# Kernel tuning notes

Measured on AMD Instinct MI355X. Metric: run time of the kernel, lower is better.

Reference implementation:

```python
import jax, jax.numpy as jnp
import numpy as np

B, T_PREV, T_CUR = 256, 128, 129
N_COV, N_TREAT, N_CONF = 30, 57, 5
H, FC = 128, 128
D_IN = N_COV + N_TREAT            # 87, lstm external input size
D_CELL = D_IN + N_CONF            # 92, cell input = [x_t, z_{t-1}]


def setup_inputs() -> dict:
    key = jax.random.key(0)
    ks = jax.random.split(key, 18)
    s = 0.05
    return {
        "previous_covariates": jax.random.normal(ks[0], (B, T_PREV, N_COV), jnp.float32),
        "previous_treatments": jax.random.normal(ks[1], (B, T_PREV, N_TREAT), jnp.float32),
        "current_covariates": jax.random.normal(ks[2], (B, T_CUR, N_COV), jnp.float32),
        "init_input": jax.random.normal(ks[3], (1, 1, D_IN), jnp.float32) * s,
        "h0": jax.random.normal(ks[4], (1, H), jnp.float32) * s,
        "c0": jax.random.normal(ks[5], (1, H), jnp.float32) * s,
        "z0": jax.random.normal(ks[6], (1, N_CONF), jnp.float32) * s,
        "W_ih": jax.random.normal(ks[7], (4 * H, D_CELL), jnp.float32) * s,
        "W_hh": jax.random.normal(ks[8], (4 * H, H), jnp.float32) * s,
        "b_ih": jax.random.normal(ks[9], (4 * H,), jnp.float32) * s,
        "b_hh": jax.random.normal(ks[10], (4 * H,), jnp.float32) * s,
        "W_z": jax.random.normal(ks[11], (N_CONF, H), jnp.float32) * s,
        "b_z": jax.random.normal(ks[12], (N_CONF,), jnp.float32) * s,
        "dec_W1": jax.random.normal(ks[13], (N_TREAT, N_COV + N_CONF, FC), jnp.float32) * s,
        "dec_b1": jax.random.normal(ks[14], (N_TREAT, FC), jnp.float32) * s,
        "dec_W2": jax.random.normal(ks[15], (N_TREAT, FC), jnp.float32) * s,
        "dec_b2": jax.random.normal(ks[16], (N_TREAT,), jnp.float32) * s,
    }


def _forward(previous_covariates, previous_treatments, current_covariates,
             init_input, h0, c0, z0, W_ih, W_hh, b_ih, b_hh, W_z, b_z,
             dec_W1, dec_b1, dec_W2, dec_b2):
    Bn = previous_covariates.shape[0]
    # (T_PREV, B, D_IN)
    x = jnp.concatenate([previous_covariates, previous_treatments], -1).transpose(1, 0, 2)
    # prepend trainable init input -> (T_CUR, B, D_IN)
    rnn_in = jnp.concatenate([jnp.broadcast_to(init_input, (1, Bn, D_IN)), x], 0)

    bias = b_ih + b_hh

    def step(carry, xt):
        h, c, z = carry
        inp = jnp.concatenate([xt, z], -1)                 # (B, D_CELL)
        gates = inp @ W_ih.T + h @ W_hh.T + bias           # (B, 4H)
        i, f, g, o = jnp.split(gates, 4, axis=-1)          # torch LSTMCell gate order
        c = jax.nn.sigmoid(f) * c + jax.nn.sigmoid(i) * jnp.tanh(g)
        h = jax.nn.sigmoid(o) * jnp.tanh(c)
        z = h @ W_z.T + b_z                                # (B, N_CONF)
        return (h, c, z), z

    carry0 = (jnp.broadcast_to(h0, (Bn, H)),
              jnp.broadcast_to(c0, (Bn, H)),
              jnp.broadcast_to(z0, (Bn, N_CONF)))
    _, zs = jax.lax.scan(step, carry0, rnn_in)             # (T_CUR, B, N_CONF)

    hidden_confounders = zs.reshape(-1, N_CONF)            # (T_CUR*B, N_CONF)
    covariates = current_covariates.transpose(1, 0, 2).reshape(-1, N_COV)
    # shapes match by construction (T_CUR*B rows each) -> no pad branch
    multitask_input = jnp.concatenate([hidden_confounders, covariates], -1)  # (N, 35)

    # batched per-treatment Linear -> LeakyReLU(0.01) -> Linear
    hdec = jax.nn.leaky_relu(
        jnp.einsum('nc,tcf->ntf', multitask_input, dec_W1) + dec_b1, 0.01)
    preds = jnp.einsum('ntf,tf->nt', hdec, dec_W2) + dec_b2                   # (N, 57)

    # T_CUR*B % (T_PREV) == 0 with these shapes -> no element trim
    confounders = hidden_confounders.reshape(T_PREV, -1, N_CONF)              # (128, 258, 5)
    return preds, confounders


def reference(previous_covariates, previous_treatments, current_covariates,
              init_input, h0, c0, z0, W_ih, W_hh, b_ih, b_hh, W_z, b_z,
              dec_W1, dec_b1, dec_W2, dec_b2):
    return _forward(previous_covariates, previous_treatments, current_covariates,
                    init_input, h0, c0, z0, W_ih, W_hh, b_ih, b_hh, W_z, b_z,
                    dec_W1, dec_b1, dec_W2, dec_b2)
```

## Files before the change

### kernel.cpp

```cpp
#include <hip/hip_runtime.h>
#include <stdint.h>

#define BATCH 256
#define T_PREVN 128
#define T_CURN 129
#define N_COV 30
#define N_TREAT 57
#define N_CONF 5
#define HID 128
#define D_IN 87
#define D_CELL 92
#define GATES 512
#define PRED_N (T_CURN*BATCH)
#define CONF_OFF (PRED_N*N_TREAT)

#define OFF_W1   0
#define SZ_W1    (57*8*2*64*8*2)
#define OFF_WIH  SZ_W1
#define SZ_WIH   (32*3*64*8*2)
#define OFF_GX   (OFF_W1 + SZ_W1 + SZ_WIH)
#define SZ_GX    (PRED_N*512*2)
#define OFF_MT   (OFF_GX + SZ_GX)
#define SZ_MT    (PRED_N*40*2)
#define WS_GX    (OFF_MT + SZ_MT)
#define WS_NEED  SZ_W1
#define WS_NEED2 (SZ_W1 + SZ_MT)

typedef _Float16 h2 __attribute__((ext_vector_type(2)));
typedef _Float16 h4 __attribute__((ext_vector_type(4)));
typedef _Float16 h8 __attribute__((ext_vector_type(8)));
typedef float f32x4 __attribute__((ext_vector_type(4)));

__device__ inline float rcp_fast(float x){
#if __has_builtin(__builtin_amdgcn_rcpf)
    return __builtin_amdgcn_rcpf(x);
#else
    return 1.0f / x;
#endif
}
__device__ inline float sigmoid_f(float x){ return rcp_fast(1.0f + __expf(-x)); }
__device__ inline float tanh_f(float x){ return 1.0f - 2.0f*rcp_fast(1.0f + __expf(2.0f*x)); }

__device__ inline float dot2f(h2 a, h2 b, float c){
#if __has_builtin(__builtin_amdgcn_fdot2)
    return __builtin_amdgcn_fdot2(a, b, c, false);
#else
    return c + (float)a.x*(float)b.x + (float)a.y*(float)b.y;
#endif
}
__device__ inline unsigned short f2us(float v){
    _Float16 h = (_Float16)v;
    return __builtin_bit_cast(unsigned short, h);
}
__device__ inline h2 us2h2(unsigned int u){
    return __builtin_bit_cast(h2, u);
}

__global__ __launch_bounds__(256) void prep_all(
    const float* __restrict__ dW1, const float* __restrict__ W_ih,
    const float* __restrict__ cc,
    _Float16* __restrict__ wsh, _Float16* __restrict__ wihf,
    _Float16* __restrict__ mT)
{
    const int bid = blockIdx.x;
    if (bid < 228){
        const int tid = bid*256 + threadIdx.x;
        const int treat = tid >> 10;
        const int r     = tid & 1023;
        const int ft    = r >> 7;
        const int ks    = (r >> 6) & 1;
        const int l     = r & 63;
        const int col   = ft*16 + (l & 15);
        const int kb    = ks*32 + ((l >> 4) << 3);
        h8 v;
        #pragma unroll
        for (int j = 0; j < 8; j++){
            const int k = kb + j;
            v[j] = (k < 35) ? (_Float16)dW1[(treat*35 + k)*128 + col] : (_Float16)0.0f;
        }
        *(h8*)(wsh + (size_t)tid*8) = v;
    } else if (bid < 252){
        const int tid = (bid - 228)*256 + threadIdx.x;
        const int ct  = tid / 192;
        const int rem = tid - ct*192;
        const int ks  = rem >> 6;
        const int l   = rem & 63;
        const int gate = ct*16 + (l & 15);
        const int kb   = ks*32 + ((l >> 4) << 3);
        h8 v;
        #pragma unroll
        for (int j = 0; j < 8; j++){
            const int k = kb + j;
            v[j] = (k < D_IN) ? (_Float16)W_ih[gate*D_CELL + k] : (_Float16)0.0f;
        }
        *(h8*)(wihf + (size_t)tid*8) = v;
    } else {
        const int idx = (bid - 252)*256 + threadIdx.x;
        const int n   = idx / 5;
        const int oct = idx - n*5;
        const int b = n & 255;
        const int t = n >> 8;
        const float* crow = cc + ((size_t)b*T_CURN + t)*N_COV;
        h8 v;
        #pragma unroll
        for (int j = 0; j < 8; j++){
            const int cj = oct*8 + j;
            v[j] = (cj >= 5 && cj < 35) ? (_Float16)crow[cj - 5] : (_Float16)0.0f;
        }
        *(h8*)(mT + (size_t)n*40 + oct*8) = v;
    }
}

__global__ __launch_bounds__(256, 2) void gx_gemm(
    const float* __restrict__ pc, const float* __restrict__ pt,
    const float* __restrict__ init_input,
    const _Float16* __restrict__ wihf, _Float16* __restrict__ Gx)
{
    __shared__ alignas(16) _Float16 a_lds[64*104];
    __shared__ alignas(16) _Float16 gx_lds[64*264];

    const int tid = threadIdx.x;
    const int nb  = blockIdx.x * 64;

    for (int idx = tid; idx < 64*96; idx += 256){
        const int r = idx / 96;
        const int k = idx - r*96;
        const int n = nb + r;
        const int bb = n / 129;
        const int t  = n - bb*129;
        float v = 0.0f;
        if (k < D_IN){
            if (t == 0) v = init_input[k];
            else        v = (k < N_COV) ? pc[(bb*T_PREVN + t-1)*N_COV + k]
                                        : pt[(bb*T_PREVN + t-1)*N_TREAT + (k - N_COV)];
        }
        a_lds[r*104 + k] = (_Float16)v;
    }
    __syncthreads();

    const int w    = tid >> 6;
    const int l    = tid & 63;
    const int col  = l & 15;
    const int quad = l >> 4;

    const _Float16* ar = a_lds + (w*16 + col)*104 + quad*8;
    const h8 a0 = *(const h8*)(ar);
    const h8 a1 = *(const h8*)(ar + 32);
    const h8 a2 = *(const h8*)(ar + 64);

    for (int half = 0; half < 2; half++){
        #pragma unroll
        for (int ct8 = 0; ct8 < 16; ct8++){
            const int ct = half*16 + ct8;
            const _Float16* bp = wihf + (size_t)ct*1536 + l*8;
            const h8 b0 = *(const h8*)(bp);
            const h8 b1 = *(const h8*)(bp + 512);
            const h8 b2 = *(const h8*)(bp + 1024);
            f32x4 acc = {0.f, 0.f, 0.f, 0.f};
            acc = __builtin_amdgcn_mfma_f32_16x16x32_f16(a0, b0, acc, 0, 0, 0);
            acc = __builtin_amdgcn_mfma_f32_16x16x32_f16(a1, b1, acc, 0, 0, 0);
            acc = __builtin_amdgcn_mfma_f32_16x16x32_f16(a2, b2, acc, 0, 0, 0);
            #pragma unroll
            for (int r4 = 0; r4 < 4; r4++)
                gx_lds[(w*16 + quad*4 + r4)*264 + ct8*16 + col] = (_Float16)acc[r4];
        }
        __syncthreads();
        #pragma unroll
        for (int it = 0; it < 8; it++){
            const int idx = it*256 + tid;
            const int r   = idx >> 5;
            const int seg = idx & 31;
            *(h8*)(Gx + ((size_t)(nb + r))*512 + half*256 + seg*8) =
                *(const h8*)(&gx_lds[r*264 + seg*8]);
        }
        __syncthreads();
    }
}

__global__ __launch_bounds__(1024, 4) void lstm_scan_oct(
    const float* __restrict__ h0, const float* __restrict__ c0,
    const float* __restrict__ z0,
    const float* __restrict__ W_ih, const float* __restrict__ W_hh,
    const float* __restrict__ b_ih, const float* __restrict__ b_hh,
    const float* __restrict__ W_z, const float* __restrict__ b_z,
    const _Float16* __restrict__ Gx,
    float* __restrict__ zs_out, _Float16* __restrict__ mT)
{
    const int b   = blockIdx.x;
    const int tid = threadIdx.x;
    const int u   = tid >> 3;
    const int r   = tid & 7;
    const int gsel = r >> 1;
    const int gate_l = (gsel << 7) + u;

    __shared__ alignas(16) unsigned short v16h[2][128];
    __shared__ alignas(16) unsigned short hall[T_CURN*136];
    __shared__ alignas(16) unsigned short gxc[2][16*512];
    __shared__ alignas(16) float wzf[5*HID];
    __shared__ alignas(16) _Float16 wz16[5*HID];
    __shared__ float z0c[5];

    for (int i = tid; i < 5*HID; i += 1024){
        const float v = W_z[i];
        wzf[i]  = v;
        wz16[i] = (_Float16)v;
    }
    if (tid < HID) v16h[0][tid] = f2us(h0[tid]);
    if (tid < 5){
        float acc0 = 0.0f, acc1 = 0.0f;
        #pragma unroll 8
        for (int k = 0; k < HID; k += 2){
            acc0 += W_z[tid*HID + k]     * h0[k];
            acc1 += W_z[tid*HID + k + 1] * h0[k + 1];
        }
        z0c[tid] = z0[tid] - b_z[tid] - (acc0 + acc1);
    }
    {
        const int row = tid >> 6;
        const uint4 p = *(const uint4*)(Gx + ((size_t)b*T_CURN + row)*512 + (size_t)(tid & 63)*8);
        *(uint4*)(&gxc[0][(row << 9) + (tid & 63)*8]) = p;
    }
    __syncthreads();

    const int kbase = r << 4;
    h2 wi_[8], wf_[8], wg_[8], wo_[8];
    {
        float zA[5], zB[5], zC[5], zD[5];
        #pragma unroll
// ... 91 lines not shown

        gval += (t == 0) ? b0_l : be_l;
        gval += (float)*(const _Float16*)(&gxc[cb][((t & 15) << 9) + gate_l]);

        const float earg = (gsel == 2) ? (2.0f*gval) : (-gval);
        const float e = __expf(earg);
        const float dd = rcp_fast(1.0f + e);
        const float av = (gsel == 2) ? (1.0f - 2.0f*dd) : dd;

        const float v1 = __shfl_xor(av, 2);
        const float v2 = __shfl_xor(av, 4);
        const float v3 = __shfl_xor(v1, 4);
        float si, sf, tg, so;
        if (gsel == 0){ si = av; sf = v1; tg = v2; so = v3; }
        else if (gsel == 1){ si = v1; sf = av; tg = v3; so = v2; }
        else if (gsel == 2){ si = v2; sf = v3; tg = av; so = v1; }
        else              { si = v3; sf = v2; tg = v1; so = av; }

        c = sf*c + si*tg;
        const float h = so * tanh_f(c);

        if (r == 0){
            const unsigned short hu = f2us(h);
            v16h[(t + 1) & 1][u] = hu;
            hall[t*136 + u] = hu;
        }
        if (pok)
            *(uint4*)(&gxc[cb ^ 1][((tid >> 6) << 9) + (tid & 63)*8]) = pre;
        __syncthreads();
    }

    for (int idx = tid; idx < T_CURN*N_CONF; idx += 1024){
        const int t  = idx / 5;
        const int zi = idx - t*5;
        const uint4* hr = (const uint4*)(hall + t*136);
        const uint4* wr = (const uint4*)(wz16 + zi*HID);
        float s0 = 0.f, s1 = 0.f;
        #pragma unroll
        for (int i = 0; i < 16; i++){
            const uint4 hq = hr[i];
            const uint4 wq = wr[i];
            s0 = dot2f(us2h2(hq.x), us2h2(wq.x), s0);
            s1 = dot2f(us2h2(hq.y), us2h2(wq.y), s1);
            s0 = dot2f(us2h2(hq.z), us2h2(wq.z), s0);
            s1 = dot2f(us2h2(hq.w), us2h2(wq.w), s1);
        }
        const float z = s0 + s1 + b_z[zi];
        const int n = t*BATCH + b;
        zs_out[(size_t)n*N_CONF + zi] = z;
        if (mT) mT[(size_t)n*40 + zi] = (_Float16)z;
    }
}

__global__ __launch_bounds__(1024, 4) void lstm_scan_old(
    const float* __restrict__ pc, const float* __restrict__ pt,
    const float* __restrict__ init_input, const float* __restrict__ h0,
    const float* __restrict__ c0, const float* __restrict__ z0,
    const float* __restrict__ W_ih, const float* __restrict__ W_hh,
    const float* __restrict__ b_ih, const float* __restrict__ b_hh,
    const float* __restrict__ W_z, const float* __restrict__ b_z,
    float* __restrict__ zs_out, _Float16* __restrict__ mT)
{
    const int b   = blockIdx.x;
    const int tid = threadIdx.x;
    const int g   = tid >> 1;
    const int hf  = tid & 1;

    __shared__ alignas(16) unsigned short v16[224];
    __shared__ alignas(16) unsigned short xall[T_CURN*88];
    __shared__ alignas(16) unsigned short hall[T_CURN*136];
    __shared__ alignas(16) float gbuf[GATES];
    __shared__ alignas(16) _Float16 wz16[5*HID];
    __shared__ float z0c[5];

    float wzg[5];
    #pragma unroll
    for (int z = 0; z < 5; z++) wzg[z] = W_ih[g*D_CELL + 87 + z];

    float be = b_ih[g] + b_hh[g];
    #pragma unroll
    for (int z = 0; z < 5; z++) be += wzg[z] * b_z[z];

    h2 w[56];
    if (hf == 0){
        #pragma unroll
        for (int i = 0; i < 43; i++){
            h2 p; p.x = (_Float16)W_ih[g*D_CELL + 2*i];
                  p.y = (_Float16)W_ih[g*D_CELL + 2*i + 1];
            w[i] = p;
        }
        { h2 p; p.x = (_Float16)W_ih[g*D_CELL + 86]; p.y = (_Float16)0.0f; w[43] = p; }
        #pragma unroll
        for (int i = 44; i < 56; i++){
            const int u = 2*(i - 44);
            float f0 = W_hh[g*HID + u], f1 = W_hh[g*HID + u + 1];
            #pragma unroll
            for (int z = 0; z < 5; z++){
                f0 += wzg[z]*W_z[z*HID + u];
                f1 += wzg[z]*W_z[z*HID + u + 1];
            }
            h2 p; p.x = (_Float16)f0; p.y = (_Float16)f1;
            w[i] = p;
        }
    } else {
        #pragma unroll
        for (int i = 0; i < 52; i++){
            const int u = 24 + 2*i;
            float f0 = W_hh[g*HID + u], f1 = W_hh[g*HID + u + 1];
            #pragma unroll
            for (int z = 0; z < 5; z++){
                f0 += wzg[z]*W_z[z*HID + u];
                f1 += wzg[z]*W_z[z*HID + u + 1];
            }
            h2 p; p.x = (_Float16)f0; p.y = (_Float16)f1;
            w[i] = p;
        }
        #pragma unroll
        for (int i = 52; i < 56; i++){ h2 p; p.x=(_Float16)0.f; p.y=(_Float16)0.f; w[i]=p; }
    }

    for (int idx = tid; idx < T_CURN*88; idx += 1024){
        const int row = idx / 88;
        const int col = idx - row*88;
        float v = 0.0f;
        if (col < D_IN){
            if (row == 0) v = init_input[col];
            else {
                const int tp = row - 1;
                v = (col < N_COV) ? pc[(b*T_PREVN + tp)*N_COV + col]
                                  : pt[(b*T_PREVN + tp)*N_TREAT + (col - N_COV)];
            }
        }
        xall[idx] = f2us(v);
    }

    float c = 0.0f;
    if (tid < HID){ v16[88 + tid] = f2us(h0[tid]); c = c0[tid]; }
    if (tid >= 216 && tid < 224) v16[tid] = 0;

    if (tid < 5){
        float acc0 = 0.0f, acc1 = 0.0f;
        #pragma unroll 8
        for (int u = 0; u < HID; u += 2){
            acc0 += W_z[tid*HID + u]     * h0[u];
            acc1 += W_z[tid*HID + u + 1] * h0[u + 1];
        }
        z0c[tid] = z0[tid] - b_z[tid] - (acc0 + acc1);
    }
    __syncthreads();

    if (tid >= 128 && tid < 216) v16[tid - 128] = xall[tid - 128];
    float b0 = be;
    #pragma unroll
    for (int z = 0; z < 5; z++) b0 += wzg[z] * z0c[z];
    __syncthreads();

    const unsigned short* vbase = v16 + hf*112;
    for (int t = 0; t < T_CURN; t++){
        float a0 = 0.f, a1 = 0.f, a2 = 0.f, a3 = 0.f;
        #pragma unroll
        for (int i = 0; i < 14; i++){
            const uint4 q = *(const uint4*)(vbase + i*8);
            a0 = dot2f(w[4*i+0], us2h2(q.x), a0);
            a1 = dot2f(w[4*i+1], us2h2(q.y), a1);
            a2 = dot2f(w[4*i+2], us2h2(q.z), a2);
            a3 = dot2f(w[4*i+3], us2h2(q.w), a3);
        }
        float s = (a0 + a1) + (a2 + a3);
        s += __shfl_xor(s, 1);
        if (hf == 0) gbuf[g] = s + ((t == 0) ? b0 : be);
        __syncthreads();

        if (tid < HID){
            const float gi = gbuf[tid];
            const float gf = gbuf[128 + tid];
            const float gg = gbuf[256 + tid];
            const float go = gbuf[384 + tid];
            c = sigmoid_f(gf)*c + sigmoid_f(gi)*tanh_f(gg);
            const float h = sigmoid_f(go)*tanh_f(c);
            const unsigned short hu = f2us(h);
            v16[88 + tid] = hu;
            hall[t*136 + tid] = hu;
        } else if (tid < 216){
            if (t < T_PREVN) v16[tid - 128] = xall[(t + 1)*88 + (tid - 128)];
        }
        __syncthreads();
    }

    for (int i = tid; i < 5*HID; i += 1024) wz16[i] = (_Float16)W_z[i];
    __syncthreads();

    if (tid < T_CURN*N_CONF){
        const int t  = tid / 5;
        const int zi = tid - t*5;
        const uint4* hr = (const uint4*)(hall + t*136);
        const uint4* wr = (const uint4*)(wz16 + zi*HID);
        float a0 = 0.f, a1 = 0.f;
        #pragma unroll
        for (int i = 0; i < 16; i++){
            const uint4 hq = hr[i];
            const uint4 wq = wr[i];
            a0 = dot2f(us2h2(hq.x), us2h2(wq.x), a0);
            a1 = dot2f(us2h2(hq.y), us2h2(wq.y), a1);
            a0 = dot2f(us2h2(hq.z), us2h2(wq.z), a0);
            a1 = dot2f(us2h2(hq.w), us2h2(wq.w), a1);
        }
        const float z = a0 + a1 + b_z[zi];
        const int n = t*BATCH + b;
        zs_out[(size_t)n*N_CONF + zi] = z;
        if (mT) mT[(size_t)n*40 + zi] = (_Float16)z;
    }
}

__global__ __launch_bounds__(256) void prepack_w1(const float* __restrict__ dW1,
                                                  _Float16* __restrict__ wsh)
{
    const int tid = blockIdx.x*256 + threadIdx.x;
    const int treat = tid >> 10;
    const int r     = tid & 1023;
    const int ft    = r >> 7;
    const int ks    = (r >> 6) & 1;
    const int l     = r & 63;
    const int col   = ft*16 + (l & 15);
    const int kb    = ks*32 + ((l >> 4) << 3);
    h8 v;
    #pragma unroll
    for (int j = 0; j < 8; j++){
        const int k = kb + j;
        v[j] = (k < 35) ? (_Float16)dW1[(treat*35 + k)*128 + col] : (_Float16)0.0f;
    }
    *(h8*)(wsh + (size_t)tid*8) = v;
}

__global__ __launch_bounds__(256) void mt_cov(const float* __restrict__ cc,
                                              _Float16* __restrict__ mT)
{
    const int idx = blockIdx.x*256 + threadIdx.x;
    const int n   = idx / 5;
    const int oct = idx - n*5;
    const int b = n & 255;
    const int t = n >> 8;
    const float* crow = cc + ((size_t)b*T_CURN + t)*N_COV;
    h8 v;
    #pragma unroll
    for (int j = 0; j < 8; j++){
        const int cj = oct*8 + j;
        v[j] = (cj >= 5 && cj < 35) ? (_Float16)crow[cj - 5] : (_Float16)0.0f;
    }
    *(h8*)(mT + (size_t)n*40 + oct*8) = v;
}

__global__ __launch_bounds__(256, 2) void decoder_treat(
    const _Float16* __restrict__ mT, const _Float16* __restrict__ wsh,
    const float* __restrict__ db1, const float* __restrict__ dW2,
    const float* __restrict__ db2, float* __restrict__ preds)
{
    const int treat = blockIdx.x;
    const int rg    = blockIdx.y;
    const int w     = threadIdx.x >> 6;
    const int l     = threadIdx.x & 63;
    const int q     = l >> 4;
    const int r16   = l & 15;

    h8 bf0[8], bf1[8];
    const _Float16* bp = wsh + (size_t)treat*8192 + l*8;
    #pragma unroll
    for (int ft = 0; ft < 8; ft++){
        bf0[ft] = *(const h8*)(bp + ft*1024);
        bf1[ft] = *(const h8*)(bp + ft*1024 + 512);
    }
    float b1r[8], w2r[8], w2c[8];
    #pragma unroll
    for (int ft = 0; ft < 8; ft++){
        b1r[ft] = db1[treat*128 + ft*16 + r16];
        w2r[ft] = dW2[treat*128 + ft*16 + r16];
        w2c[ft] = 0.01f * w2r[ft];
    }
    const float b2 = db2[treat];

    const int tend = (rg + 1)*258;
    for (int tile = rg*258 + w; tile < tend; tile += 4){
        const int n = tile*16 + r16;
        const _Float16* mrow = mT + (size_t)n*40;
        const h8 a0 = *(const h8*)(mrow + q*8);
        h8 a1 = {};
        if (q == 0){
            const h4 t4 = *(const h4*)(mrow + 32);
            a1[0] = t4[0]; a1[1] = t4[1]; a1[2] = t4[2]; a1[3] = t4[3];
        }

        f32x4 pred = {0.f, 0.f, 0.f, 0.f};
        #pragma unroll
        for (int ft = 0; ft < 8; ft++){
            f32x4 acc = {b1r[ft], b1r[ft], b1r[ft], b1r[ft]};
            acc = __builtin_amdgcn_mfma_f32_16x16x32_f16(a0, bf0[ft], acc, 0, 0, 0);
            acc = __builtin_amdgcn_mfma_f32_16x16x32_f16(a1, bf1[ft], acc, 0, 0, 0);
            #pragma unroll
            for (int r = 0; r < 4; r++){
                const float a  = acc[r];
                const float mx = fmaxf(a, 0.0f);
                const float mn = fminf(a, 0.0f);
                pred[r] += mx*w2r[ft] + mn*w2c[ft];
            }
        }
        #pragma unroll
        for (int r = 0; r < 4; r++){
            float s = pred[r];
            s += __shfl_xor(s, 1);
            s += __shfl_xor(s, 2);
            s += __shfl_xor(s, 4);
            s += __shfl_xor(s, 8);
            pred[r] = s;
        }
        if (r16 == 0){
            #pragma unroll
            for (int r = 0; r < 4; r++)
                preds[(size_t)(tile*16 + q*4 + r)*N_TREAT + treat] = pred[r] + b2;
        }
    }
}

__global__ __launch_bounds__(256) void decoder_mfma(
    const float* __restrict__ cc, const float* __restrict__ zs,
    const _Float16* __restrict__ wsh,
    const float* __restrict__ db1, const float* __restrict__ dW2,
    const float* __restrict__ db2, float* __restrict__ preds)
{
    __shared__ alignas(16) _Float16 m_lds[64*72];

    const int tid  = threadIdx.x;
    const int base = blockIdx.x * 64;
    const int t    = base >> 8;

    for (int idx = tid; idx < 64*72; idx += 256){
        const int r = idx / 72;
        const int j = idx - r*72;
        const int n = base + r;
        const int b = n & 255;
        float v = 0.0f;
        if (j < 5)       v = zs[n*N_CONF + j];
        else if (j < 35) v = cc[(b*T_CURN + t)*N_COV + (j - 5)];
        m_lds[r*72 + j] = (_Float16)v;
    }
    __syncthreads();

    const int w    = tid >> 6;
    const int l    = tid & 63;
    const int row  = l & 15;
    const int quad = l >> 4;

    const _Float16* arow = m_lds + (w*16 + row)*72 + quad*8;
    const h8 a0 = *(const h8*)(arow);
    const h8 a1 = *(const h8*)(arow + 32);
    const int nbase = base + w*16 + quad*4;

    for (int treat = 0; treat < 57; treat++){
        const _Float16* bp = wsh + (size_t)treat*8192 + l*8;
        f32x4 pred = {0.0f, 0.0f, 0.0f, 0.0f};
        #pragma unroll
        for (int ft = 0; ft < 8; ft++){
            const h8 b0 = *(const h8*)(bp + ft*1024);
            const h8 b1 = *(const h8*)(bp + ft*1024 + 512);
            f32x4 acc = {0.0f, 0.0f, 0.0f, 0.0f};
            acc = __builtin_amdgcn_mfma_f32_16x16x32_f16(a0, b0, acc, 0, 0, 0);
            acc = __builtin_amdgcn_mfma_f32_16x16x32_f16(a1, b1, acc, 0, 0, 0);
            const int col = ft*16 + row;
            const float hb1 = db1[treat*128 + col];
            const float hw2 = dW2[treat*128 + col];
            #pragma unroll
            for (int r = 0; r < 4; r++){
                float hd = acc[r] + hb1;
                hd = (hd > 0.0f) ? hd : 0.01f*hd;
                pred[r] += hd * hw2;
            }
        }
        #pragma unroll
        for (int r = 0; r < 4; r++){
            float s = pred[r];
            s += __shfl_xor(s, 1);
            s += __shfl_xor(s, 2);
            s += __shfl_xor(s, 4);
            s += __shfl_xor(s, 8);
            pred[r] = s;
        }
        if (row == 0){
            const float b2 = db2[treat];
            #pragma unroll
            for (int r = 0; r < 4; r++)
                preds[(size_t)(nbase + r)*N_TREAT + treat] = pred[r] + b2;
        }
    }
}

__global__ __launch_bounds__(256) void decoder_fallback(
    const float* __restrict__ cc, const float* __restrict__ zs,
    const float* __restrict__ dW1, const float* __restrict__ db1,
    const float* __restrict__ dW2, const float* __restrict__ db2,
    float* __restrict__ preds)
{
    const int t     = blockIdx.x;
    const int treat = blockIdx.y;
    const int tid   = threadIdx.x;

    __shared__ alignas(16) float w1t[128*36];
    __shared__ float b1s[128];
    __shared__ float w2s[128];

    for (int it = tid; it < 35*128; it += 256){
        const int cidx = it >> 7;
        const int f    = it & 127;
        w1t[f*36 + cidx] = dW1[(treat*35 + cidx)*128 + f];
    }
    if (tid < 128){
        b1s[tid] = db1[treat*128 + tid];
        w2s[tid] = dW2[treat*128 + tid];
        w1t[tid*36 + 35] = 0.0f;
    }
    __syncthreads();

    const int n = t*BATCH + tid;
    float m[36];
    #pragma unroll
    for (int j = 0; j < N_CONF; j++) m[j] = zs[n*N_CONF + j];
    #pragma unroll
    for (int j = 0; j < N_COV; j++)  m[N_CONF + j] = cc[(tid*T_CURN + t)*N_COV + j];
    m[35] = 0.0f;

    const float b2 = db2[treat];
    float pred = 0.0f;
    for (int f = 0; f < 128; f++){
        float a = b1s[f];
        const float4* wr = (const float4*)(w1t + f*36);
        #pragma unroll
        for (int cq = 0; cq < 9; cq++){
            const float4 v = wr[cq];
            a += m[cq*4+0]*v.x + m[cq*4+1]*v.y + m[cq*4+2]*v.z + m[cq*4+3]*v.w;
        }
        a = (a > 0.0f) ? a : 0.01f*a;
        pred += a * w2s[f];
    }
    preds[n*N_TREAT + treat] = pred + b2;
}

extern "C" void kernel_launch(void* const* d_in, const int* in_sizes, int n_in,
                              void* d_out, int out_size, void* d_ws, size_t ws_size,
                              hipStream_t stream)
{
    const float* pc   = (const float*)d_in[0];
    const float* pt   = (const float*)d_in[1];
    const float* cc   = (const float*)d_in[2];
    const float* init = (const float*)d_in[3];
    const float* h0   = (const float*)d_in[4];
    const float* c0   = (const float*)d_in[5];
    const float* z0   = (const float*)d_in[6];
    const float* W_ih = (const float*)d_in[7];
    const float* W_hh = (const float*)d_in[8];
    const float* b_ih = (const float*)d_in[9];
    const float* b_hh = (const float*)d_in[10];
    const float* W_z  = (const float*)d_in[11];
    const float* b_z  = (const float*)d_in[12];
    const float* dW1  = (const float*)d_in[13];
    const float* db1  = (const float*)d_in[14];
    const float* dW2  = (const float*)d_in[15];
    const float* db2  = (const float*)d_in[16];

    float* preds = (float*)d_out;
    float* zs    = (float*)d_out + CONF_OFF;

    if (ws_size >= (size_t)WS_GX){
        _Float16* wsh  = (_Float16*)d_ws;
        _Float16* wihf = (_Float16*)((char*)d_ws + OFF_WIH);
        _Float16* Gx   = (_Float16*)((char*)d_ws + OFF_GX);
        _Float16* mT   = (_Float16*)((char*)d_ws + OFF_MT);

        prep_all<<<897, 256, 0, stream>>>(dW1, W_ih, cc, wsh, wihf, mT);
        gx_gemm<<<516, 256, 0, stream>>>(pc, pt, init, wihf, Gx);
        lstm_scan_oct<<<BATCH, 1024, 0, stream>>>(h0, c0, z0, W_ih, W_hh,
                                                  b_ih, b_hh, W_z, b_z, Gx, zs, mT);
        decoder_treat<<<dim3(N_TREAT, 8), 256, 0, stream>>>(mT, wsh, db1, dW2, db2, preds);
    } else if (ws_size >= (size_t)WS_NEED2){
        _Float16* wsh = (_Float16*)d_ws;
        _Float16* mT  = (_Float16*)((char*)d_ws + WS_NEED);
        prepack_w1<<<228, 256, 0, stream>>>(dW1, wsh);
        mt_cov<<<645, 256, 0, stream>>>(cc, mT);
        lstm_scan_old<<<BATCH, 1024, 0, stream>>>(pc, pt, init, h0, c0, z0,
                                                  W_ih, W_hh, b_ih, b_hh, W_z, b_z, zs, mT);
        decoder_treat<<<dim3(N_TREAT, 8), 256, 0, stream>>>(mT, wsh, db1, dW2, db2, preds);
    } else if (ws_size >= (size_t)WS_NEED){
        _Float16* wsh = (_Float16*)d_ws;
        prepack_w1<<<228, 256, 0, stream>>>(dW1, wsh);
        lstm_scan_old<<<BATCH, 1024, 0, stream>>>(pc, pt, init, h0, c0, z0,
                                                  W_ih, W_hh, b_ih, b_hh, W_z, b_z,
                                                  zs, (_Float16*)nullptr);
        decoder_mfma<<<516, 256, 0, stream>>>(cc, zs, wsh, db1, dW2, db2, preds);
    } else {
        lstm_scan_old<<<BATCH, 1024, 0, stream>>>(pc, pt, init, h0, c0, z0,
                                                  W_ih, W_hh, b_ih, b_hh, W_z, b_z,
                                                  zs, (_Float16*)nullptr);
        decoder_fallback<<<dim3(T_CURN, N_TREAT), 256, 0, stream>>>(
            cc, zs, dW1, db1, dW2, db2, preds);
    }
}
```

Baseline: 233.0 us.

## Batch 16 sequences per block in LSTM scan using MFMA recurrence

Adds an LSTM scan kernel in which each block processes 16 batch rows and computes the recurrent h·W_eff product with MFMA. The input gate contributions from Gx are prefetched through a triple-buffered LDS ring, and z is computed by an extra MFMA on one wave. Bias and initial-confounder terms are folded into the Gx GEMM epilogue, and W_eff plus W_z are prepacked into fragment layout in prep_all. Only 16 blocks are launched instead of 256, which trades parallelism across CUs for tensor-core throughput on the serial recurrence.

```diff
diff --git a/kernel.cpp b/kernel.cpp
--- a/kernel.cpp
+++ b/kernel.cpp
@@ -23,6 +23,11 @@
 #define OFF_MT   (OFF_GX + SZ_GX)
 #define SZ_MT    (PRED_N*40*2)
 #define WS_GX    (OFF_MT + SZ_MT)
+#define OFF_WEFF WS_GX
+#define SZ_WEFF  (32*4*64*8*2)
+#define OFF_WZF  (OFF_WEFF + SZ_WEFF)
+#define SZ_WZF   (4*64*8*2)
+#define WS_MF    (OFF_WZF + SZ_WZF)
 #define WS_NEED  SZ_W1
 #define WS_NEED2 (SZ_W1 + SZ_MT)
 
@@ -58,9 +63,11 @@
 
 __global__ __launch_bounds__(256) void prep_all(
     const float* __restrict__ dW1, const float* __restrict__ W_ih,
-    const float* __restrict__ cc,
+    const float* __restrict__ cc, const float* __restrict__ W_hh,
+    const float* __restrict__ W_z,
     _Float16* __restrict__ wsh, _Float16* __restrict__ wihf,
-    _Float16* __restrict__ mT)
+    _Float16* __restrict__ mT, _Float16* __restrict__ weff,
+    _Float16* __restrict__ wzfr)
 {
     const int bid = blockIdx.x;
     if (bid < 228){
@@ -94,7 +101,7 @@
             v[j] = (k < D_IN) ? (_Float16)W_ih[gate*D_CELL + k] : (_Float16)0.0f;
         }
         *(h8*)(wihf + (size_t)tid*8) = v;
-    } else {
+    } else if (bid < 897){
         const int idx = (bid - 252)*256 + threadIdx.x;
         const int n   = idx / 5;
         const int oct = idx - n*5;
@@ -108,16 +115,58 @@
             v[j] = (cj >= 5 && cj < 35) ? (_Float16)crow[cj - 5] : (_Float16)0.0f;
         }
         *(h8*)(mT + (size_t)n*40 + oct*8) = v;
+    } else if (bid < 929){
+        const int idx = (bid - 897)*256 + threadIdx.x;
+        const int mk  = idx >> 6;
+        const int l   = idx & 63;
+        const int m   = mk >> 2;
+        const int ks  = mk & 3;
+        const int rowp = m*16 + (l & 15);
+        const int u   = rowp >> 2;
+        const int gi  = rowp & 3;
+        const int g   = gi*128 + u;
+        const int kb  = ks*32 + ((l >> 4) << 3);
+        float wz[5];
+        #pragma unroll
+        for (int z = 0; z < 5; z++) wz[z] = W_ih[g*D_CELL + D_IN + z];
+        h8 v;
+        #pragma unroll
+        for (int j = 0; j < 8; j++){
+            const int k = kb + j;
+            float f = W_hh[g*HID + k];
+            #pragma unroll
+            for (int z = 0; z < 5; z++) f += wz[z]*W_z[z*HID + k];
+            v[j] = (_Float16)f;
+        }
+        *(h8*)(weff + (size_t)idx*8) = v;
+    } else {
+        const int t2 = threadIdx.x;
+        const int ks = t2 >> 6;
+        const int l  = t2 & 63;
+        const int row = l & 15;
+        const int kb  = ks*32 + ((l >> 4) << 3);
+        h8 v;
+        #pragma unroll
+        for (int j = 0; j < 8; j++)
+            v[j] = (row < 5) ? (_Float16)W_z[row*HID + kb + j] : (_Float16)0.0f;
+        *(h8*)(wzfr + (size_t)t2*8) = v;
     }
 }
 
 __global__ __launch_bounds__(256, 2) void gx_gemm(
     const float* __restrict__ pc, const float* __restrict__ pt,
     const float* __restrict__ init_input,
-    const _Float16* __restrict__ wihf, _Float16* __restrict__ Gx)
+    const _Float16* __restrict__ wihf, _Float16* __restrict__ Gx,
+    const float* __restrict__ W_ih, const float* __restrict__ W_z,
+    const float* __restrict__ b_ih, const float* __restrict__ b_hh,
+    const float* __restrict__ b_z, const float* __restrict__ h0,
+    const float* __restrict__ z0, const int fold_bias)
 {
     __shared__ alignas(16) _Float16 a_lds[64*104];
     __shared__ alignas(16) _Float16 gx_lds[64*264];
+    __shared__ float be_lds[512];
+    __shared__ float d0_lds[512];
+    __shared__ float z0c[5];
 
     const int tid = threadIdx.x;
     const int nb  = blockIdx.x * 64;
@@ -136,7 +185,29 @@
         }
         a_lds[r*104 + k] = (_Float16)v;
     }
+    if (fold_bias && tid < 5){
+        float a0 = 0.f, a1 = 0.f;
+        #pragma unroll 8
+        for (int k = 0; k < HID; k += 2){
+            a0 += W_z[tid*HID + k]     * h0[k];
+            a1 += W_z[tid*HID + k + 1] * h0[k + 1];
+        }
+        z0c[tid] = z0[tid] - b_z[tid] - (a0 + a1);
+    }
     __syncthreads();
+    if (fold_bias){
+        for (int g = tid; g < 512; g += 256){
+            float w0v = W_ih[g*D_CELL + D_IN + 0];
+            float w1v = W_ih[g*D_CELL + D_IN + 1];
+            float w2v = W_ih[g*D_CELL + D_IN + 2];
+            float w3v = W_ih[g*D_CELL + D_IN + 3];
+            float w4v = W_ih[g*D_CELL + D_IN + 4];
+            be_lds[g] = b_ih[g] + b_hh[g]
+                      + w0v*b_z[0] + w1v*b_z[1] + w2v*b_z[2] + w3v*b_z[3] + w4v*b_z[4];
+            d0_lds[g] = w0v*z0c[0] + w1v*z0c[1] + w2v*z0c[2] + w3v*z0c[3] + w4v*z0c[4];
+        }
+        __syncthreads();
+    }
 
     const int w    = tid >> 6;
     const int l    = tid & 63;
@@ -161,8 +232,16 @@
             acc = __builtin_amdgcn_mfma_f32_16x16x32_f16(a1, b1, acc, 0, 0, 0);
             acc = __builtin_amdgcn_mfma_f32_16x16x32_f16(a2, b2, acc, 0, 0, 0);
             #pragma unroll
-            for (int r4 = 0; r4 < 4; r4++)
-                gx_lds[(w*16 + quad*4 + r4)*264 + ct8*16 + col] = (_Float16)acc[r4];
+            for (int r4 = 0; r4 < 4; r4++){
+                float val = acc[r4];
+                if (fold_bias){
+                    const int g = ct*16 + col;
+                    const int n = nb + w*16 + quad*4 + r4;
+                    val += be_lds[g];
+                    if (n % 129 == 0) val += d0_lds[g];
+                }
+                gx_lds[(w*16 + quad*4 + r4)*264 + ct8*16 + col] = (_Float16)val;
+            }
         }
         __syncthreads();
         #pragma unroll
@@ -174,6 +253,140 @@
                 *(const h8*)(&gx_lds[r*264 + seg*8]);
         }
         __syncthreads();
+    }
+}
+
+__global__ __launch_bounds__(1024, 4) void lstm_scan_mfma(
+    const float* __restrict__ h0, const float* __restrict__ c0,
+    const float* __restrict__ b_z,
+    const _Float16* __restrict__ weff, const _Float16* __restrict__ wzfr,
+    const _Float16* __restrict__ Gx,
+    float* __restrict__ zs_out, _Float16* __restrict__ mT)
+{
+    const int tid = threadIdx.x;
+    const int w   = tid >> 6;
+    const int l   = tid & 63;
+    const int col = l & 15;
+    const int q   = l >> 4;
+    const int b0  = blockIdx.x * 16;
+
+    __shared__ alignas(16) _Float16 hsw[2][16*128];
+    __shared__ alignas(16) _Float16 gxc[3][16*520];
+    __shared__ float zl[129*80];
+
+    for (int idx = tid; idx < 2048; idx += 1024){
+        const int bt = idx >> 7;
+        const int u  = idx & 127;
+        const int gp = (u >> 3) ^ (bt & 7);
+        hsw[0][bt*128 + gp*8 + (u & 7)] = (_Float16)h0[u];
+    }
+    {
+        const uint4 p = *(const uint4*)(Gx + ((size_t)(b0 + w)*T_CURN + 0)*512 + (size_t)l*8);
+        *(uint4*)(&gxc[0][w*520 + l*8]) = p;
+    }
+    uint4 preA = *(const uint4*)(Gx + ((size_t)(b0 + w)*T_CURN + 1)*512 + (size_t)l*8);
+
+    h8 aw0[4], aw1[4], az[4];
+    #pragma unroll
+    for (int ks = 0; ks < 4; ks++){
+        aw0[ks] = *(const h8*)(weff + (size_t)((w*4 + ks)*64 + l)*8);
+        aw1[ks] = *(const h8*)(weff + (size_t)(((w + 16)*4 + ks)*64 + l)*8);
+        az[ks]  = *(const h8*)(wzfr + (size_t)(ks*64 + l)*8);
+    }
+    const int u0 = 4*w + q;
+    const int u1 = 64 + 4*w + q;
+    float cr0 = c0[u0];
+    float cr1 = c0[u1];
+    __syncthreads();
+
+    for (int t = 0; t < T_CURN; t++){
+        const int cur  = t & 1;
+        const int g3   = t % 3;
+        uint4 preB;
+        const bool ldB = (t + 2 <= 128);
+        if (ldB)
+            preB = *(const uint4*)(Gx + ((size_t)(b0 + w)*T_CURN + (t + 2))*512 + (size_t)l*8);
+
+        f32x4 acc0 = {0.f,0.f,0.f,0.f};
+        f32x4 acc1 = {0.f,0.f,0.f,0.f};
+        f32x4 accz = {0.f,0.f,0.f,0.f};
+        #pragma unroll
+        for (int ks = 0; ks < 4; ks++){
+            const int gp = (ks*4 + q) ^ (col & 7);
+            const h8 hb = *(const h8*)(&hsw[cur][col*128 + gp*8]);
+            acc0 = __builtin_amdgcn_mfma_f32_16x16x32_f16(aw0[ks], hb, acc0, 0, 0, 0);
+            acc1 = __builtin_amdgcn_mfma_f32_16x16x32_f16(aw1[ks], hb, acc1, 0, 0, 0);
+            if (w == 15)
+                accz = __builtin_amdgcn_mfma_f32_16x16x32_f16(az[ks], hb, accz, 0, 0, 0);
+        }
+
+        float g0[4], g1[4];
+        #pragma unroll
+        for (int r = 0; r < 4; r++){
+            g0[r] = acc0[r] + (float)gxc[g3][col*520 + r*128 + u0];
+            g1[r] = acc1[r] + (float)gxc[g3][col*520 + r*128 + u1];
+        }
+        float hv0, hv1;
+        {
+            const float i_ = sigmoid_f(g0[0]);
+            const float f_ = sigmoid_f(g0[1]);
+            const float t_ = tanh_f(g0[2]);
+            const float o_ = sigmoid_f(g0[3]);
+            cr0 = f_*cr0 + i_*t_;
+            hv0 = o_ * tanh_f(cr0);
+        }
+        {
+            const float i_ = sigmoid_f(g1[0]);
+            const float f_ = sigmoid_f(g1[1]);
+            const float t_ = tanh_f(g1[2]);
+            const float o_ = sigmoid_f(g1[3]);
+            cr1 = f_*cr1 + i_*t_;
+            hv1 = o_ * tanh_f(cr1);
+        }
+        {
+            const int gp0 = (u0 >> 3) ^ (col & 7);
+            hsw[cur ^ 1][col*128 + gp0*8 + (u0 & 7)] = (_Float16)hv0;
+            const int gp1 = (u1 >> 3) ^ (col & 7);
+            hsw[cur ^ 1][col*128 + gp1*8 + (u1 & 7)] = (_Float16)hv1;
+        }
+        if (w == 15 && t > 0){
+            #pragma unroll
+            for (int r = 0; r < 4; r++){
+                const int zi = q*4 + r;
+                if (zi < 5) zl[(t - 1)*80 + zi*16 + col] = accz[r];
+            }
+        }
+        if (t + 1 <= 128)
+            *(uint4*)(&gxc[(t + 1) % 3][w*520 + l*8]) = preA;
+        if (ldB) preA = preB;
+        __syncthreads();
+    }
+
+    if (w == 15){
+        f32x4 accz = {0.f,0.f,0.f,0.f};
+        #pragma unroll
+        for (int ks = 0; ks < 4; ks++){
+            const int gp = (ks*4 + q) ^ (col & 7);
+            const h8 hb = *(const h8*)(&hsw[1][col*128 + gp*8]);
+            accz = __builtin_amdgcn_mfma_f32_16x16x32_f16(az[ks], hb, accz, 0, 0, 0);
+        }
+        #pragma unroll
+        for (int r = 0; r < 4; r++){
+            const int zi = q*4 + r;
+            if (zi < 5) zl[128*80 + zi*16 + col] = accz[r];
+        }
+    }
+    __syncthreads();
+
+    for (int idx = tid; idx < T_CURN*80; idx += 1024){
+        const int t   = idx / 80;
+        const int rem = idx - t*80;
+        const int zi  = rem >> 4;
+        const int bt  = rem & 15;
+        const float z = zl[idx] + b_z[zi];
+        const int n   = t*BATCH + b0 + bt;
+        zs_out[(size_t)n*N_CONF + zi] = z;
+        mT[(size_t)n*40 + zi] = (_Float16)z;
     }
 }
 
@@ -371,166 +584,6 @@
     }
 }
 
-__global__ __launch_bounds__(1024, 4) void lstm_scan_old(
-    const float* __restrict__ pc, const float* __restrict__ pt,
-    const float* __restrict__ init_input, const float* __restrict__ h0,
-    const float* __restrict__ c0, const float* __restrict__ z0,
-    const float* __restrict__ W_ih, const float* __restrict__ W_hh,
-    const float* __restrict__ b_ih, const float* __restrict__ b_hh,
-    const float* __restrict__ W_z, const float* __restrict__ b_z,
-    float* __restrict__ zs_out, _Float16* __restrict__ mT)
-{
-    const int b   = blockIdx.x;
-    const int tid = threadIdx.x;
-    const int g   = tid >> 1;
-    const int hf  = tid & 1;
-
-    __shared__ alignas(16) unsigned short v16[224];
-    __shared__ alignas(16) unsigned short xall[T_CURN*88];
-    __shared__ alignas(16) unsigned short hall[T_CURN*136];
-    __shared__ alignas(16) float gbuf[GATES];
-    __shared__ alignas(16) _Float16 wz16[5*HID];
-    __shared__ float z0c[5];
-
-    float wzg[5];
-    #pragma unroll
-    for (int z = 0; z < 5; z++) wzg[z] = W_ih[g*D_CELL + 87 + z];
-
-    float be = b_ih[g] + b_hh[g];
-    #pragma unroll
-    for (int z = 0; z < 5; z++) be += wzg[z] * b_z[z];
-
-    h2 w[56];
-    if (hf == 0){
-        #pragma unroll
-        for (int i = 0; i < 43; i++){
-            h2 p; p.x = (_Float16)W_ih[g*D_CELL + 2*i];
-                  p.y = (_Float16)W_ih[g*D_CELL + 2*i + 1];
-            w[i] = p;
-        }
-        { h2 p; p.x = (_Float16)W_ih[g*D_CELL + 86]; p.y = (_Float16)0.0f; w[43] = p; }
-        #pragma unroll
-        for (int i = 44; i < 56; i++){
-            const int u = 2*(i - 44);
-            float f0 = W_hh[g*HID + u], f1 = W_hh[g*HID + u + 1];
-            #pragma unroll
-            for (int z = 0; z < 5; z++){
-                f0 += wzg[z]*W_z[z*HID + u];
-                f1 += wzg[z]*W_z[z*HID + u + 1];
-            }
-            h2 p; p.x = (_Float16)f0; p.y = (_Float16)f1;
-            w[i] = p;
-        }
-    } else {
-        #pragma unroll
-        for (int i = 0; i < 52; i++){
-            const int u = 24 + 2*i;
-            float f0 = W_hh[g*HID + u], f1 = W_hh[g*HID + u + 1];
-            #pragma unroll
-            for (int z = 0; z < 5; z++){
-                f0 += wzg[z]*W_z[z*HID + u];
-                f1 += wzg[z]*W_z[z*HID + u + 1];
-            }
-            h2 p; p.x = (_Float16)f0; p.y = (_Float16)f1;
-            w[i] = p;
-        }
-        #pragma unroll
-        for (int i = 52; i < 56; i++){ h2 p; p.x=(_Float16)0.f; p.y=(_Float16)0.f; w[i]=p; }
-    }
-
-    for (int idx = tid; idx < T_CURN*88; idx += 1024){
-        const int row = idx / 88;
-        const int col = idx - row*88;
-        float v = 0.0f;
-        if (col < D_IN){
-            if (row == 0) v = init_input[col];
-            else {
-                const int tp = row - 1;
-                v = (col < N_COV) ? pc[(b*T_PREVN + tp)*N_COV + col]
-                                  : pt[(b*T_PREVN + tp)*N_TREAT + (col - N_COV)];
-            }
-        }
-        xall[idx] = f2us(v);
-    }
-
-    float c = 0.0f;
-    if (tid < HID){ v16[88 + tid] = f2us(h0[tid]); c = c0[tid]; }
-    if (tid >= 216 && tid < 224) v16[tid] = 0;
-
-    if (tid < 5){
-        float acc0 = 0.0f, acc1 = 0.0f;
-        #pragma unroll 8
-        for (int u = 0; u < HID; u += 2){
-            acc0 += W_z[tid*HID + u]     * h0[u];
-            acc1 += W_z[tid*HID + u + 1] * h0[u + 1];
-        }
-        z0c[tid] = z0[tid] - b_z[tid] - (acc0 + acc1);
-    }
-    __syncthreads();
-
-    if (tid >= 128 && tid < 216) v16[tid - 128] = xall[tid - 128];
-    float b0 = be;
-    #pragma unroll
-    for (int z = 0; z < 5; z++) b0 += wzg[z] * z0c[z];
-    __syncthreads();
-
-    const unsigned short* vbase = v16 + hf*112;
-    for (int t = 0; t < T_CURN; t++){
-        float a0 = 0.f, a1 = 0.f, a2 = 0.f, a3 = 0.f;
-        #pragma unroll
-        for (int i = 0; i < 14; i++){
-            const uint4 q = *(const uint4*)(vbase + i*8);
-            a0 = dot2f(w[4*i+0], us2h2(q.x), a0);
-            a1 = dot2f(w[4*i+1], us2h2(q.y), a1);
-            a2 = dot2f(w[4*i+2], us2h2(q.z), a2);
-            a3 = dot2f(w[4*i+3], us2h2(q.w), a3);
-        }
-        float s = (a0 + a1) + (a2 + a3);
-        s += __shfl_xor(s, 1);
-        if (hf == 0) gbuf[g] = s + ((t == 0) ? b0 : be);
-        __syncthreads();
-
-        if (tid < HID){
-            const float gi = gbuf[tid];
-            const float gf = gbuf[128 + tid];
-            const float gg = gbuf[256 + tid];
-            const float go = gbuf[384 + tid];
-            c = sigmoid_f(gf)*c + sigmoid_f(gi)*tanh_f(gg);
-            const float h = sigmoid_f(go)*tanh_f(c);
-            const unsigned short hu = f2us(h);
-            v16[88 + tid] = hu;
-            hall[t*136 + tid] = hu;
-        } else if (tid < 216){
-            if (t < T_PREVN) v16[tid - 128] = xall[(t + 1)*88 + (tid - 128)];
-        }
-        __syncthreads();
-    }
-
-    for (int i = tid; i < 5*HID; i += 1024) wz16[i] = (_Float16)W_z[i];
-    __syncthreads();
-
-    if (tid < T_CURN*N_CONF){
-        const int t  = tid / 5;
-        const int zi = tid - t*5;
-        const uint4* hr = (const uint4*)(hall + t*136);
-        const uint4* wr = (const uint4*)(wz16 + zi*HID);
-        float a0 = 0.f, a1 = 0.f;
-        #pragma unroll
-        for (int i = 0; i < 16; i++){
-            const uint4 hq = hr[i];
-            const uint4 wq = wr[i];
-            a0 = dot2f(us2h2(hq.x), us2h2(wq.x), a0);
-            a1 = dot2f(us2h2(hq.y), us2h2(wq.y), a1);
-            a0 = dot2f(us2h2(hq.z), us2h2(wq.z), a0);
-            a1 = dot2f(us2h2(hq.w), us2h2(wq.w), a1);
-        }
-        const float z = a0 + a1 + b_z[zi];
-        const int n = t*BATCH + b;
-        zs_out[(size_t)n*N_CONF + zi] = z;
-        if (mT) mT[(size_t)n*40 + zi] = (_Float16)z;
-    }
-}
-
 __global__ __launch_bounds__(256) void prepack_w1(const float* __restrict__ dW1,
                                                   _Float16* __restrict__ wsh)
 {
@@ -569,6 +622,166 @@
     *(h8*)(mT + (size_t)n*40 + oct*8) = v;
 }
 
+__global__ __launch_bounds__(1024, 4) void lstm_scan_old(
+    const float* __restrict__ pc, const float* __restrict__ pt,
+    const float* __restrict__ init_input, const float* __restrict__ h0,
+    const float* __restrict__ c0, const float* __restrict__ z0,
+    const float* __restrict__ W_ih, const float* __restrict__ W_hh,
+    const float* __restrict__ b_ih, const float* __restrict__ b_hh,
+    const float* __restrict__ W_z, const float* __restrict__ b_z,
+    float* __restrict__ zs_out, _Float16* __restrict__ mT)
+{
+    const int b   = blockIdx.x;
+    const int tid = threadIdx.x;
+    const int g   = tid >> 1;
+    const int hf  = tid & 1;
+
+    __shared__ alignas(16) unsigned short v16[224];
+    __shared__ alignas(16) unsigned short xall[T_CURN*88];
+    __shared__ alignas(16) unsigned short hall[T_CURN*136];
+    __shared__ alignas(16) float gbuf[GATES];
+    __shared__ alignas(16) _Float16 wz16[5*HID];
+    __shared__ float z0c[5];
+
+    float wzg[5];
+    #pragma unroll
+    for (int z = 0; z < 5; z++) wzg[z] = W_ih[g*D_CELL + 87 + z];
+
+    float be = b_ih[g] + b_hh[g];
+    #pragma unroll
+    for (int z = 0; z < 5; z++) be += wzg[z] * b_z[z];
+
+    h2 w[56];
+    if (hf == 0){
+        #pragma unroll
+        for (int i = 0; i < 43; i++){
+            h2 p; p.x = (_Float16)W_ih[g*D_CELL + 2*i];
+                  p.y = (_Float16)W_ih[g*D_CELL + 2*i + 1];
+            w[i] = p;
+        }
+        { h2 p; p.x = (_Float16)W_ih[g*D_CELL + 86]; p.y = (_Float16)0.0f; w[43] = p; }
+        #pragma unroll
+        for (int i = 44; i < 56; i++){
+            const int u = 2*(i - 44);
+            float f0 = W_hh[g*HID + u], f1 = W_hh[g*HID + u + 1];
+            #pragma unroll
+            for (int z = 0; z < 5; z++){
+                f0 += wzg[z]*W_z[z*HID + u];
+                f1 += wzg[z]*W_z[z*HID + u + 1];
+            }
+            h2 p; p.x = (_Float16)f0; p.y = (_Float16)f1;
+            w[i] = p;
+        }
+    } else {
+        #pragma unroll
+        for (int i = 0; i < 52; i++){
+            const int u = 24 + 2*i;
+            float f0 = W_hh[g*HID + u], f1 = W_hh[g*HID + u + 1];
+            #pragma unroll
+            for (int z = 0; z < 5; z++){
+                f0 += wzg[z]*W_z[z*HID + u];
+                f1 += wzg[z]*W_z[z*HID + u + 1];
+            }
+            h2 p; p.x = (_Float16)f0; p.y = (_Float16)f1;
+            w[i] = p;
+        }
+        #pragma unroll
+        for (int i = 52; i < 56; i++){ h2 p; p.x=(_Float16)0.f; p.y=(_Float16)0.f; w[i]=p; }
+    }
+
+    for (int idx = tid; idx < T_CURN*88; idx += 1024){
+        const int row = idx / 88;
+        const int col = idx - row*88;
+        float v = 0.0f;
+        if (col < D_IN){
+            if (row == 0) v = init_input[col];
+            else {
+                const int tp = row - 1;
+                v = (col < N_COV) ? pc[(b*T_PREVN + tp)*N_COV + col]
+                                  : pt[(b*T_PREVN + tp)*N_TREAT + (col - N_COV)];
+            }
+        }
+        xall[idx] = f2us(v);
+    }
+
+    float c = 0.0f;
+    if (tid < HID){ v16[88 + tid] = f2us(h0[tid]); c = c0[tid]; }
+    if (tid >= 216 && tid < 224) v16[tid] = 0;
+
+    if (tid < 5){
+        float acc0 = 0.0f, acc1 = 0.0f;
+        #pragma unroll 8
+        for (int u = 0; u < HID; u += 2){
+            acc0 += W_z[tid*HID + u]     * h0[u];
+            acc1 += W_z[tid*HID + u + 1] * h0[u + 1];
+        }
+        z0c[tid] = z0[tid] - b_z[tid] - (acc0 + acc1);
+    }
+    __syncthreads();
+
+    if (tid >= 128 && tid < 216) v16[tid - 128] = xall[tid - 128];
+    float b0 = be;
+    #pragma unroll
+    for (int z = 0; z < 5; z++) b0 += wzg[z] * z0c[z];
+    __syncthreads();
+
+    const unsigned short* vbase = v16 + hf*112;
+    for (int t = 0; t < T_CURN; t++){
+        float a0 = 0.f, a1 = 0.f, a2 = 0.f, a3 = 0.f;
+        #pragma unroll
+        for (int i = 0; i < 14; i++){
+            const uint4 q = *(const uint4*)(vbase + i*8);
+            a0 = dot2f(w[4*i+0], us2h2(q.x), a0);
+            a1 = dot2f(w[4*i+1], us2h2(q.y), a1);
+            a2 = dot2f(w[4*i+2], us2h2(q.z), a2);
+            a3 = dot2f(w[4*i+3], us2h2(q.w), a3);
+        }
+        float s = (a0 + a1) + (a2 + a3);
+        s += __shfl_xor(s, 1);
+        if (hf == 0) gbuf[g] = s + ((t == 0) ? b0 : be);
+        __syncthreads();
+
+        if (tid < HID){
+            const float gi = gbuf[tid];
+            const float gf = gbuf[128 + tid];
+            const float gg = gbuf[256 + tid];
+            const float go = gbuf[384 + tid];
+            c = sigmoid_f(gf)*c + sigmoid_f(gi)*tanh_f(gg);
+            const float h = sigmoid_f(go)*tanh_f(c);
+            const unsigned short hu = f2us(h);
+            v16[88 + tid] = hu;
+            hall[t*136 + tid] = hu;
+        } else if (tid < 216){
+            if (t < T_PREVN) v16[tid - 128] = xall[(t + 1)*88 + (tid - 128)];
+        }
+        __syncthreads();
+    }
+
+    for (int i = tid; i < 5*HID; i += 1024) wz16[i] = (_Float16)W_z[i];
+    __syncthreads();
+
+    if (tid < T_CURN*N_CONF){
+        const int t  = tid / 5;
+        const int zi = tid - t*5;
+        const uint4* hr = (const uint4*)(hall + t*136);
+        const uint4* wr = (const uint4*)(wz16 + zi*HID);
+        float a0 = 0.f, a1 = 0.f;
+        #pragma unroll
+        for (int i = 0; i < 16; i++){
+            const uint4 hq = hr[i];
+            const uint4 wq = wr[i];
+            a0 = dot2f(us2h2(hq.x), us2h2(wq.x), a0);
+            a1 = dot2f(us2h2(hq.y), us2h2(wq.y), a1);
+            a0 = dot2f(us2h2(hq.z), us2h2(wq.z), a0);
+            a1 = dot2f(us2h2(hq.w), us2h2(wq.w), a1);
+        }
+        const float z = a0 + a1 + b_z[zi];
+        const int n = t*BATCH + b;
+        zs_out[(size_t)n*N_CONF + zi] = z;
+        if (mT) mT[(size_t)n*40 + zi] = (_Float16)z;
+    }
+}
+
 __global__ __launch_bounds__(256, 2) void decoder_treat(
     const _Float16* __restrict__ mT, const _Float16* __restrict__ wsh,
     const float* __restrict__ db1, const float* __restrict__ dW2,
@@ -635,78 +848,6 @@
             #pragma unroll
             for (int r = 0; r < 4; r++)
                 preds[(size_t)(tile*16 + q*4 + r)*N_TREAT + treat] = pred[r] + b2;
-        }
-    }
-}
-
-__global__ __launch_bounds__(256) void decoder_mfma(
-    const float* __restrict__ cc, const float* __restrict__ zs,
-    const _Float16* __restrict__ wsh,
-    const float* __restrict__ db1, const float* __restrict__ dW2,
-    const float* __restrict__ db2, float* __restrict__ preds)
-{
-    __shared__ alignas(16) _Float16 m_lds[64*72];
-
-    const int tid  = threadIdx.x;
-    const int base = blockIdx.x * 64;
-    const int t    = base >> 8;
-
-    for (int idx = tid; idx < 64*72; idx += 256){
-        const int r = idx / 72;
-        const int j = idx - r*72;
-        const int n = base + r;
-        const int b = n & 255;
-        float v = 0.0f;
-        if (j < 5)       v = zs[n*N_CONF + j];
-        else if (j < 35) v = cc[(b*T_CURN + t)*N_COV + (j - 5)];
-        m_lds[r*72 + j] = (_Float16)v;
-    }
-    __syncthreads();
-
-    const int w    = tid >> 6;
-    const int l    = tid & 63;
-    const int row  = l & 15;
-    const int quad = l >> 4;
-
-    const _Float16* arow = m_lds + (w*16 + row)*72 + quad*8;
-    const h8 a0 = *(const h8*)(arow);
-    const h8 a1 = *(const h8*)(arow + 32);
-    const int nbase = base + w*16 + quad*4;
-
-    for (int treat = 0; treat < 57; treat++){
-        const _Float16* bp = wsh + (size_t)treat*8192 + l*8;
-        f32x4 pred = {0.0f, 0.0f, 0.0f, 0.0f};
-        #pragma unroll
-        for (int ft = 0; ft < 8; ft++){
-            const h8 b0 = *(const h8*)(bp + ft*1024);
-            const h8 b1 = *(const h8*)(bp + ft*1024 + 512);
-            f32x4 acc = {0.0f, 0.0f, 0.0f, 0.0f};
-            acc = __builtin_amdgcn_mfma_f32_16x16x32_f16(a0, b0, acc, 0, 0, 0);
-            acc = __builtin_amdgcn_mfma_f32_16x16x32_f16(a1, b1, acc, 0, 0, 0);
-            const int col = ft*16 + row;
-            const float hb1 = db1[treat*128 + col];
-            const float hw2 = dW2[treat*128 + col];
-            #pragma unroll
-            for (int r = 0; r < 4; r++){
-                float hd = acc[r] + hb1;
-                hd = (hd > 0.0f) ? hd : 0.01f*hd;
-                pred[r] += hd * hw2;
-            }
-        }
-        #pragma unroll
-        for (int r = 0; r < 4; r++){
-            float s = pred[r];
-            s += __shfl_xor(s, 1);
-            s += __shfl_xor(s, 2);
-            s += __shfl_xor(s, 4);
-            s += __shfl_xor(s, 8);
-            pred[r] = s;
-        }
-        if (row == 0){
-            const float b2 = db2[treat];
-            #pragma unroll
-            for (int r = 0; r < 4; r++)
-                preds[(size_t)(nbase + r)*N_TREAT + treat] = pred[r] + b2;
         }
     }
 }
@@ -786,14 +927,31 @@
     float* preds = (float*)d_out;
     float* zs    = (float*)d_out + CONF_OFF;
 
-    if (ws_size >= (size_t)WS_GX){
+    if (ws_size >= (size_t)WS_MF){
         _Float16* wsh  = (_Float16*)d_ws;
         _Float16* wihf = (_Float16*)((char*)d_ws + OFF_WIH);
         _Float16* Gx   = (_Float16*)((char*)d_ws + OFF_GX);
         _Float16* mT   = (_Float16*)((char*)d_ws + OFF_MT);
-
-        prep_all<<<897, 256, 0, stream>>>(dW1, W_ih, cc, wsh, wihf, mT);
-        gx_gemm<<<516, 256, 0, stream>>>(pc, pt, init, wihf, Gx);
+        _Float16* weff = (_Float16*)((char*)d_ws + OFF_WEFF);
+        _Float16* wzfr = (_Float16*)((char*)d_ws + OFF_WZF);
+
+        prep_all<<<930, 256, 0, stream>>>(dW1, W_ih, cc, W_hh, W_z,
+                                          wsh, wihf, mT, weff, wzfr);
+        gx_gemm<<<516, 256, 0, stream>>>(pc, pt, init, wihf, Gx,
+                                         W_ih, W_z, b_ih, b_hh, b_z, h0, z0, 1);
+        lstm_scan_mfma<<<16, 1024, 0, stream>>>(h0, c0, b_z, weff, wzfr, Gx, zs, mT);
+        decoder_treat<<<dim3(N_TREAT, 8), 256, 0, stream>>>(mT, wsh, db1, dW2, db2, preds);
+    } else if (ws_size >= (size_t)WS_GX){
+        _Float16* wsh  = (_Float16*)d_ws;
+        _Float16* wihf = (_Float16*)((char*)d_ws + OFF_WIH);
+        _Float16* Gx   = (_Float16*)((char*)d_ws + OFF_GX);
+        _Float16* mT   = (_Float16*)((char*)d_ws + OFF_MT);
+
+        prep_all<<<897, 256, 0, stream>>>(dW1, W_ih, cc, W_hh, W_z,
+                                          wsh, wihf, mT, (_Float16*)nullptr,
+                                          (_Float16*)nullptr);
+        gx_gemm<<<516, 256, 0, stream>>>(pc, pt, init, wihf, Gx,
+                                         W_ih, W_z, b_ih, b_hh, b_z, h0, z0, 0);
         lstm_scan_oct<<<BATCH, 1024, 0, stream>>>(h0, c0, z0, W_ih, W_hh,
                                                   b_ih, b_hh, W_z, b_z, Gx, zs, mT);
         decoder_treat<<<dim3(N_TREAT, 8), 256, 0, stream>>>(mT, wsh, db1, dW2, db2, preds);
@@ -805,13 +963,6 @@
         lstm_scan_old<<<BATCH, 1024, 0, stream>>>(pc, pt, init, h0, c0, z0,
                                                   W_ih, W_hh, b_ih, b_hh, W_z, b_z, zs, mT);
         decoder_treat<<<dim3(N_TREAT, 8), 256, 0, stream>>>(mT, wsh, db1, dW2, db2, preds);
-    } else if (ws_size >= (size_t)WS_NEED){
-        _Float16* wsh = (_Float16*)d_ws;
-        prepack_w1<<<228, 256, 0, stream>>>(dW1, wsh);
-        lstm_scan_old<<<BATCH, 1024, 0, stream>>>(pc, pt, init, h0, c0, z0,
-                                                  W_ih, W_hh, b_ih, b_hh, W_z, b_z,
-                                                  zs, (_Float16*)nullptr);
-        decoder_mfma<<<516, 256, 0, stream>>>(cc, zs, wsh, db1, dW2, db2, preds);
     } else {
         lstm_scan_old<<<BATCH, 1024, 0, stream>>>(pc, pt, init, h0, c0, z0,
                                                   W_ih, W_hh, b_ih, b_hh, W_z, b_z,
```

Result: slower. 274.1 us (+17.7%).
